# Kernel optimization log

Measured on AMD Instinct MI355X. Metric: run time of the kernel, lower is better.

Reference implementation:

```python
import jax, jax.numpy as jnp
import numpy as np

N_NODES = 100000
N_EDGES = 1600000
NODE_DIM = 3
EDGE_DIM = 32
HIDDEN = 128
OUT_DIM = 3
N_GRAPHS = 64


def _lin(key, fan_in, fan_out):
    k1, k2 = jax.random.split(key)
    s = 1.0 / np.sqrt(fan_in)
    W = jax.random.uniform(k1, (fan_in, fan_out), minval=-s, maxval=s, dtype=jnp.float32)
    b = jax.random.uniform(k2, (fan_out,), minval=-s, maxval=s, dtype=jnp.float32)
    return W, b


def setup_inputs() -> dict:
    key = jax.random.key(0)
    ks = jax.random.split(key, 16)
    x = jax.random.normal(ks[0], (N_NODES, NODE_DIM), dtype=jnp.float32)
    edge_index = jax.random.randint(ks[1], (2, N_EDGES), 0, N_NODES, dtype=jnp.int32)
    edge_attr = jax.random.normal(ks[2], (N_EDGES, EDGE_DIM), dtype=jnp.float32)
    batch = jnp.sort(jax.random.randint(ks[3], (N_NODES,), 0, N_GRAPHS, dtype=jnp.int32))
    # conv1: CGConv at channels=NODE_DIM, in = 2*NODE_DIM + EDGE_DIM
    Wf1, bf1 = _lin(ks[4], 2 * NODE_DIM + EDGE_DIM, NODE_DIM)
    Ws1, bs1 = _lin(ks[5], 2 * NODE_DIM + EDGE_DIM, NODE_DIM)
    Wp, bp = _lin(ks[6], NODE_DIM, HIDDEN)
    # two hidden CGConvs at channels=HIDDEN
    Wf2, bf2 = _lin(ks[7], 2 * HIDDEN + EDGE_DIM, HIDDEN)
    Ws2, bs2 = _lin(ks[8], 2 * HIDDEN + EDGE_DIM, HIDDEN)
    Wf3, bf3 = _lin(ks[9], 2 * HIDDEN + EDGE_DIM, HIDDEN)
    Ws3, bs3 = _lin(ks[10], 2 * HIDDEN + EDGE_DIM, HIDDEN)
    W1, b1 = _lin(ks[11], HIDDEN, HIDDEN)
    W2, b2 = _lin(ks[12], HIDDEN, OUT_DIM)
    return dict(x=x, edge_index=edge_index, edge_attr=edge_attr, batch=batch,
                Wf1=Wf1, bf1=bf1, Ws1=Ws1, bs1=bs1, Wp=Wp, bp=bp,
                Wf2=Wf2, bf2=bf2, Ws2=Ws2, bs2=bs2,
                Wf3=Wf3, bf3=bf3, Ws3=Ws3, bs3=bs3,
                W1=W1, b1=b1, W2=W2, b2=b2)


def _cgconv(x, src, dst, edge_attr, Wf, bf, Ws, bs):
    # z = [x_i (target), x_j (source), e_ij]; message = sigmoid(lin_f(z)) * softplus(lin_s(z))
    z = jnp.concatenate([x[dst], x[src], edge_attr], axis=-1)  # [E, 2C+F]
    m = jax.nn.sigmoid(z @ Wf + bf) * jax.nn.softplus(z @ Ws + bs)  # [E, C]
    agg = jax.ops.segment_sum(m, dst, num_segments=x.shape[0])
    return x + agg


def reference(x, edge_index, edge_attr, batch,
              Wf1, bf1, Ws1, bs1, Wp, bp,
              Wf2, bf2, Ws2, bs2, Wf3, bf3, Ws3, bs3,
              W1, b1, W2, b2):
    src, dst = edge_index[0], edge_index[1]
    h = _cgconv(x, src, dst, edge_attr, Wf1, bf1, Ws1, bs1)
    h = jax.nn.relu(h @ Wp + bp)
    h = jax.nn.relu(_cgconv(h, src, dst, edge_attr, Wf2, bf2, Ws2, bs2))
    h = jax.nn.relu(_cgconv(h, src, dst, edge_attr, Wf3, bf3, Ws3, bs3))
    # global mean pool over graphs
    sums = jax.ops.segment_sum(h, batch, num_segments=N_GRAPHS)
    counts = jax.ops.segment_sum(jnp.ones((h.shape[0],), h.dtype), batch, num_segments=N_GRAPHS)
    pooled = sums / jnp.maximum(counts, 1.0)[:, None]
    g = jax.nn.relu(pooled @ W1 + b1)
    return g @ W2 + b2
```

## Files before the change

### kernel.cpp

```cpp
#include <hip/hip_runtime.h>
#include <hip/hip_bf16.h>


#define N_NODES 100000
#define N_EDGES 1600000
#define HID 128
#define SCAN_BLOCKS 391

typedef unsigned int uint;
typedef short bf16x8 __attribute__((ext_vector_type(8)));
typedef float f32x4 __attribute__((ext_vector_type(4)));

__device__ inline float bflo(uint u) { return __uint_as_float(u << 16); }
__device__ inline float bfhi(uint u) { return __uint_as_float(u & 0xffff0000u); }
__device__ inline uint pack_bf16_2(float a, float b) {
  uint ua = __float_as_uint(a), ub = __float_as_uint(b);
  ua = (ua + 0x7fffu + ((ua >> 16) & 1u)) >> 16;
  ub = (ub + 0x7fffu + ((ub >> 16) & 1u)) >> 16;
  return ua | (ub << 16);
}
__device__ inline float sigmoidf_(float x) {
  return __builtin_amdgcn_rcpf(1.f + __expf(-x));
}
__device__ inline float softplusf_(float x) {
  return fmaxf(x, 0.f) + __logf(1.f + __expf(-fabsf(x)));
}

__global__ __launch_bounds__(256) void hist_k(const int* __restrict__ ei,
                                              int* __restrict__ deg) {
  int e = blockIdx.x * 256 + threadIdx.x;
  if (e >= N_EDGES) return;
  atomicAdd(&deg[ei[N_EDGES + e]], 1);
}

__global__ __launch_bounds__(256) void scan1_k(const int* __restrict__ deg,
                                               int* __restrict__ rowptr,
                                               int* __restrict__ bsums) {
  __shared__ int s[256];
  int i = blockIdx.x * 256 + threadIdx.x;
  int v = (i < N_NODES) ? deg[i] : 0;
  s[threadIdx.x] = v;
  __syncthreads();
  for (int off = 1; off < 256; off <<= 1) {
    int t = (threadIdx.x >= off) ? s[threadIdx.x - off] : 0;
    __syncthreads();
    s[threadIdx.x] += t;
    __syncthreads();
  }
  if (i < N_NODES) rowptr[i] = s[threadIdx.x] - v;
  if (threadIdx.x == 255) bsums[blockIdx.x] = s[255];
}

__global__ __launch_bounds__(512) void scan2_k(int* __restrict__ bsums) {
  __shared__ int s[512];
  int t = threadIdx.x;
  int v = (t < SCAN_BLOCKS) ? bsums[t] : 0;
  s[t] = v;
  __syncthreads();
  for (int off = 1; off < 512; off <<= 1) {
    int x = (t >= off) ? s[t - off] : 0;
    __syncthreads();
    s[t] += x;
    __syncthreads();
  }
  if (t < SCAN_BLOCKS) bsums[t] = s[t] - v;
}

__global__ __launch_bounds__(256) void scan3_k(int* __restrict__ rowptr,
                                               const int* __restrict__ bsums,
                                               int* __restrict__ cur) {
  int i = blockIdx.x * 256 + threadIdx.x;
  if (i < N_NODES) {
    int r = rowptr[i] + bsums[blockIdx.x];
    rowptr[i] = r;
    cur[i] = r;
  }
  if (i == 0) rowptr[N_NODES] = N_EDGES;
}

__global__ __launch_bounds__(256) void scatter_k(const int* __restrict__ ei,
                                                 int* __restrict__ cur,
                                                 uint4* __restrict__ csr) {
  int e = blockIdx.x * 256 + threadIdx.x;
  if (e >= N_EDGES) return;
  int d = ei[N_EDGES + e];
  int pos = atomicAdd(&cur[d], 1);
  csr[pos] = make_uint4((uint)ei[e], (uint)e, (uint)d, 0u);
}

__global__ __launch_bounds__(256) void ea_pack(const float* __restrict__ ea,
                                               const uint4* __restrict__ csr,
                                               uint4* __restrict__ eab) {
  long long t = (long long)blockIdx.x * 256 + threadIdx.x;
  int p = (int)(t >> 2), q = (int)(t & 3);
  if (p >= N_EDGES) return;
  uint e = csr[p].y;
  const float4* er = (const float4*)(ea + (long long)e * 32 + q * 8);
  float4 a0 = er[0], a1 = er[1];
  uint4 pk;
  pk.x = pack_bf16_2(a0.x, a0.y);
  pk.y = pack_bf16_2(a0.z, a0.w);
  pk.z = pack_bf16_2(a1.x, a1.y);
  pk.w = pack_bf16_2(a1.z, a1.w);
  eab[(long long)p * 4 + q] = pk;
}

__global__ __launch_bounds__(256) void conv1_edge(
    const float* __restrict__ x, const int* __restrict__ ei,
    const float* __restrict__ ea,
    const float* __restrict__ Wf, const float* __restrict__ bf,
    const float* __restrict__ Ws, const float* __restrict__ bs,
    float* __restrict__ agg1) {
  int e = blockIdx.x * 256 + threadIdx.x;
  if (e >= N_EDGES) return;
  int src = ei[e], dst = ei[N_EDGES + e];
  float z[38];
#pragma unroll
  for (int k = 0; k < 3; ++k) z[k] = x[dst * 3 + k];
#pragma unroll
  for (int k = 0; k < 3; ++k) z[3 + k] = x[src * 3 + k];
  const float4* er4 = (const float4*)(ea + (long long)e * 32);
#pragma unroll
  for (int k = 0; k < 8; ++k) {
    float4 v = er4[k];
    z[6 + 4 * k + 0] = v.x;
    z[6 + 4 * k + 1] = v.y;
    z[6 + 4 * k + 2] = v.z;
    z[6 + 4 * k + 3] = v.w;
  }
#pragma unroll
  for (int c = 0; c < 3; ++c) {
    float f = bf[c], s = bs[c];
#pragma unroll
    for (int k = 0; k < 38; ++k) {
      f = fmaf(z[k], Wf[k * 3 + c], f);
      s = fmaf(z[k], Ws[k * 3 + c], s);
    }
    atomicAdd(&agg1[dst * 3 + c], sigmoidf_(f) * softplusf_(s));
  }
}

__global__ __launch_bounds__(256) void proj2(
    const float* __restrict__ x, const float* __restrict__ agg1,
    const float* __restrict__ Wp, const float* __restrict__ bp,
    float* __restrict__ h, uint* __restrict__ hb) {
  long long i = (long long)blockIdx.x * 256 + threadIdx.x;
  if (i >= (long long)N_NODES * 64) return;
  int n = (int)(i >> 6), jp = (int)(i & 63);
  int j0 = jp * 2;
  float v0 = x[n * 3 + 0] + agg1[n * 3 + 0];
  float v1 = x[n * 3 + 1] + agg1[n * 3 + 1];
  float v2 = x[n * 3 + 2] + agg1[n * 3 + 2];
  float a0 = bp[j0], a1 = bp[j0 + 1];
  a0 = fmaf(v0, Wp[0 * HID + j0], a0);
  a0 = fmaf(v1, Wp[1 * HID + j0], a0);
  a0 = fmaf(v2, Wp[2 * HID + j0], a0);
  a1 = fmaf(v0, Wp[0 * HID + j0 + 1], a1);
  a1 = fmaf(v1, Wp[1 * HID + j0 + 1], a1);
  a1 = fmaf(v2, Wp[2 * HID + j0 + 1], a1);
  a0 = fmaxf(a0, 0.f);
  a1 = fmaxf(a1, 0.f);
  *(float2*)&h[(long long)n * HID + j0] = make_float2(a0, a1);
  hb[(long long)n * 64 + jp] = pack_bf16_2(a0, a1);
}

__global__ __launch_bounds__(256) void w_prep2(const float* __restrict__ Wf,
                                               const float* __restrict__ Ws,
                                               uint* __restrict__ Wpk) {
  int row = blockIdx.x * 256 + threadIdx.x;
  int pm = row >> 7;
  int c = row & 127;
  const float* W = (pm & 1) ? Ws : Wf;
  int rowoff = (pm >> 1) * 128;
  for (int kk = 0; kk < 64; ++kk) {
    float a = W[(rowoff + 2 * kk) * 128 + c];
    float b = W[(rowoff + 2 * kk + 1) * 128 + c];
    Wpk[row * 64 + kk] = pack_bf16_2(a, b);
  }
}

#define NG_STR 68
__global__ __launch_bounds__(256, 4) void node_gemmM(
    const uint* __restrict__ hb, const uint* __restrict__ Wpk,
    const float* __restrict__ bf, const float* __restrict__ bs,
    uint* __restrict__ Pb) {
  __shared__ uint Alds[64 * NG_STR];
  int part = blockIdx.x;
  int m0 = blockIdx.y * 64;
  int tid = threadIdx.x;
  {
    int r = tid >> 2, q = tid & 3;
    int row = m0 + r;
    uint* d = &Alds[r * NG_STR + q * 16];
    if (row < N_NODES) {
      const uint4* s4 = (const uint4*)&hb[(long long)row * 64 + q * 16];
      uint4 v0 = s4[0], v1 = s4[1], v2 = s4[2], v3 = s4[3];
      *(uint4*)(d + 0) = v0; *(uint4*)(d + 4) = v1;
      *(uint4*)(d + 8) = v2; *(uint4*)(d + 12) = v3;
    } else {
      uint4 z = make_uint4(0, 0, 0, 0);
      *(uint4*)(d + 0) = z; *(uint4*)(d + 4) = z;
      *(uint4*)(d + 8) = z; *(uint4*)(d + 12) = z;
    }
  }
  __syncthreads();
  int wave = tid >> 6, lane = tid & 63;
  int l15 = lane & 15, lq = lane >> 4;
  int arow = wave * 16 + l15;
  const uint* WpF = Wpk + (part * 2 + 0) * 128 * 64;
  const uint* WpS = Wpk + (part * 2 + 1) * 128 * 64;
  f32x4 accF[8], accS[8];
#pragma unroll
  for (int nt = 0; nt < 8; ++nt) {
    f32x4 z = {0.f, 0.f, 0.f, 0.f};
    accF[nt] = z;
    accS[nt] = z;
  }
#pragma unroll
  for (int ks = 0; ks < 4; ++ks) {
    bf16x8 afr = *(const bf16x8*)&Alds[arow * NG_STR + ks * 16 + lq * 4];
#pragma unroll
    for (int nt = 0; nt < 8; ++nt) {
      bf16x8 bF = *(const bf16x8*)&WpF[(nt * 16 + l15) * 64 + ks * 16 + lq * 4];
      bf16x8 bS = *(const bf16x8*)&WpS[(nt * 16 + l15) * 64 + ks * 16 + lq * 4];
      accF[nt] = __builtin_amdgcn_mfma_f32_16x16x32_bf16(afr, bF, accF[nt], 0, 0, 0);
      accS[nt] = __builtin_amdgcn_mfma_f32_16x16x32_bf16(afr, bS, accS[nt], 0, 0, 0);
    }
  }
#pragma unroll
  for (int nt = 0; nt < 8; ++nt) {
    int c = nt * 16 + l15;
    int pos = (nt >> 1) * 32 + l15 * 2 + (nt & 1);
    float fb = (part == 0) ? bf[c] : 0.f;
    float sb = (part == 0) ? bs[c] : 0.f;
#pragma unroll
    for (int reg = 0; reg < 4; ++reg) {
      int node = m0 + wave * 16 + lq * 4 + reg;
      if (node < N_NODES) {
        Pb[(long long)node * 256 + part * 128 + pos] =
            pack_bf16_2(accF[nt][reg] + fb, accS[nt][reg] + sb);
      }
    }
  }
}

__global__ __launch_bounds__(256) void w_prep(const float* __restrict__ Wf,
                                              const float* __restrict__ Ws,
                                              uint* __restrict__ Btg) {
  int t = threadIdx.x;
  const float* W = (t < 128) ? Wf : Ws;
  int c = t & 127;
#pragma unroll
  for (int kk = 0; kk < 16; ++kk) {
    float a = W[(256 + 2 * kk) * 128 + c];
    float b = W[(256 + 2 * kk + 1) * 128 + c];
    Btg[t * 16 + kk] = pack_bf16_2(a, b);
  }
}

#define EMSG_EB 64
#define CAP 16
__global__ __launch_bounds__(256, 7) void edge_msg(
    const uint* __restrict__ Pb, const uint* __restrict__ eab,
    const uint* __restrict__ Btg, const uint4* __restrict__ csr,
    const int* __restrict__ rowptr, float* __restrict__ h) {
  __shared__ float accL[CAP * 128];
  __shared__ int dstL[64], srcL[64], liL[64];
  __shared__ int dlist[CAP], compL[CAP];
  __shared__ int nDistS;
  int tid = threadIdx.x;
  int j0 = blockIdx.x * EMSG_EB;
#pragma unroll
  for (int i = 0; i < (CAP * 128) / 256; ++i) accL[tid + i * 256] = 0.f;
  if (tid < 64) {
    uint4 cj = csr[j0 + tid];
    int d = (int)cj.z;
    dstL[tid] = d;
    srcL[tid] = (int)cj.x;
    int dprev = __shfl_up(d, 1, 64);
    bool flag = (tid == 0) || (d != dprev);
    unsigned long long m = __ballot(flag);
    unsigned long long pre = (tid == 63) ? ~0ull : ((1ull << (tid + 1)) - 1);
    int li = __popcll(m & pre) - 1;
    liL[tid] = li;
    if (flag && li < CAP) {
      dlist[li] = d;
      int r0 = rowptr[d], r1 = rowptr[d + 1];
      compL[li] = ((r0 == j0 + tid) && (r1 <= j0 + EMSG_EB)) ? 1 : 0;
    }
    if (tid == 0) nDistS = __popcll(m);
  }
  __syncthreads();
  int wave = tid >> 6, lane = tid & 63;
  int c0w = wave * 32;
  int l15 = lane & 15, lq = lane >> 4;
  int chs0 = c0w + l15, chs1 = c0w + 16 + l15;
  int pbase = (wave << 5) + (l15 << 1);
  bf16x8 bfr0 = *(const bf16x8*)&Btg[chs0 * 16 + lq * 4];
  bf16x8 bfr1 = *(const bf16x8*)&Btg[chs1 * 16 + lq * 4];
  bf16x8 bfr2 = *(const bf16x8*)&Btg[(128 + chs0) * 16 + lq * 4];
  bf16x8 bfr3 = *(const bf16x8*)&Btg[(128 + chs1) * 16 + lq * 4];
#pragma unroll
  for (int mt = 0; mt < 4; ++mt) {
    bf16x8 afr =
        *(const bf16x8*)&eab[((long long)(j0 + mt * 16 + l15)) * 16 + lq * 4];
    f32x4 z = {0.f, 0.f, 0.f, 0.f};
    f32x4 accf0 = __builtin_amdgcn_mfma_f32_16x16x32_bf16(afr, bfr0, z, 0, 0, 0);
    f32x4 accf1 = __builtin_amdgcn_mfma_f32_16x16x32_bf16(afr, bfr1, z, 0, 0, 0);
    f32x4 accs0 = __builtin_amdgcn_mfma_f32_16x16x32_bf16(afr, bfr2, z, 0, 0, 0);
    f32x4 accs1 = __builtin_amdgcn_mfma_f32_16x16x32_bf16(afr, bfr3, z, 0, 0, 0);
    int o = mt * 16 + lq * 4;
    int dsts[4], lis[4];
#pragma unroll
    for (int reg = 0; reg < 4; ++reg) {
      dsts[reg] = dstL[o + reg];
      lis[reg] = liL[o + reg];
    }
    float mr0[4], mr1[4];
#pragma unroll
    for (int reg = 0; reg < 4; ++reg) {
      uint2 gd = *(const uint2*)&Pb[(long long)dsts[reg] * 256 + pbase];
      uint2 gs = *(const uint2*)&Pb[(long long)srcL[o + reg] * 256 + 128 + pbase];
      float f0 = accf0[reg] + bflo(gd.x) + bflo(gs.x);
      float s0 = accs0[reg] + bfhi(gd.x) + bfhi(gs.x);
      float f1 = accf1[reg] + bflo(gd.y) + bflo(gs.y);
      float s1 = accs1[reg] + bfhi(gd.y) + bfhi(gs.y);
      mr0[reg] = sigmoidf_(f0) * softplusf_(s0);
      mr1[reg] = sigmoidf_(f1) * softplusf_(s1);
    }
#pragma unroll
    for (int cp = 0; cp < 2; ++cp) {
      int c = (cp ? chs1 : chs0);
      const float* mr = cp ? mr1 : mr0;
      float racc = mr[0];
      int cl = lis[0], cd = dsts[0];
#pragma unroll
      for (int reg = 1; reg < 4; ++reg) {
        if (lis[reg] == cl) {
          racc += mr[reg];
        } else {
          if (cl < CAP) atomicAdd(&accL[cl * 128 + c], racc);
          else atomicAdd(&h[(long long)cd * HID + c], racc);
          cl = lis[reg]; cd = dsts[reg]; racc = mr[reg];
        }
      }
      if (cl < CAP) atomicAdd(&accL[cl * 128 + c], racc);
      else atomicAdd(&h[(long long)cd * HID + c], racc);
    }
  }
  __syncthreads();
  int nD = nDistS;
  if (nD > CAP) nD = CAP;
  int c = tid & 127;
  for (int li = tid >> 7; li < nD; li += 2) {
    int d = dlist[li];
    float v = accL[li * 128 + c];
    float* hp = &h[(long long)d * HID + c];
    if (compL[li]) {
      *hp = fmaxf(*hp + v, 0.f);
    } else {
      atomicAdd(hp, v);
    }
  }
}

__global__ __launch_bounds__(256) void relu2(float* __restrict__ h,
                                             uint* __restrict__ hb) {
  const int total = N_NODES * 32;
  for (int i = blockIdx.x * 256 + threadIdx.x; i < total; i += gridDim.x * 256) {
    float4 v = ((float4*)h)[i];
    v.x = fmaxf(v.x, 0.f); v.y = fmaxf(v.y, 0.f);
    v.z = fmaxf(v.z, 0.f); v.w = fmaxf(v.w, 0.f);
    ((float4*)h)[i] = v;
    uint2 o;
    o.x = pack_bf16_2(v.x, v.y);
    o.y = pack_bf16_2(v.z, v.w);
    *(uint2*)&hb[(long long)i * 2] = o;
  }
}

__global__ __launch_bounds__(256) void relu_k(float* __restrict__ h) {
  const int total = N_NODES * HID / 4;
  for (int i = blockIdx.x * 256 + threadIdx.x; i < total; i += gridDim.x * 256) {
    float4 v = ((float4*)h)[i];
    v.x = fmaxf(v.x, 0.f); v.y = fmaxf(v.y, 0.f);
    v.z = fmaxf(v.z, 0.f); v.w = fmaxf(v.w, 0.f);
    ((float4*)h)[i] = v;
  }
}

#define POOL_NODES 128
__global__ __launch_bounds__(128) void pool2(
    const float* __restrict__ h, const int* __restrict__ batch,
    float* __restrict__ sums, float* __restrict__ cnts) {
  int n0 = blockIdx.x * POOL_NODES;
  if (n0 >= N_NODES) return;
  int t = threadIdx.x;
  int nEnd = n0 + POOL_NODES;
  if (nEnd > N_NODES) nEnd = N_NODES;
  float acc = 0.f;
  int bcur = batch[n0];
  int cnt = 0;
  for (int n = n0; n < nEnd; ++n) {
    int b = batch[n];
    if (b != bcur) {
      atomicAdd(&sums[bcur * HID + t], acc);
      if (t == 0) atomicAdd(&cnts[bcur], (float)cnt);
      acc = 0.f; cnt = 0; bcur = b;
    }
    acc += h[(long long)n * HID + t];
    ++cnt;
  }
  atomicAdd(&sums[bcur * HID + t], acc);
  if (t == 0) atomicAdd(&cnts[bcur], (float)cnt);
}

__global__ __launch_bounds__(128) void mlpA(
    const float* __restrict__ sums, const float* __restrict__ cnts,
    const float* __restrict__ W1, const float* __restrict__ b1,
    float* __restrict__ g) {
  __shared__ float pl[HID];
  int gr = blockIdx.x, j = threadIdx.x;
  float cnt = fmaxf(cnts[gr], 1.f);
  pl[j] = sums[gr * HID + j] / cnt;
  __syncthreads();
  float acc = b1[j];
#pragma unroll 8
  for (int k = 0; k < HID; ++k) acc = fmaf(pl[k], W1[k * HID + j], acc);
  g[gr * HID + j] = fmaxf(acc, 0.f);
}

__global__ __launch_bounds__(256) void mlpB(
    const float* __restrict__ g, const float* __restrict__ W2,
    const float* __restrict__ b2, float* __restrict__ out) {
  int t = threadIdx.x;
  if (t >= 64 * 3) return;
  int gr = t / 3, o = t % 3;
  float acc = b2[o];
#pragma unroll 8
  for (int k = 0; k < HID; ++k) acc = fmaf(g[gr * HID + k], W2[k * 3 + o], acc);
  out[t] = acc;
}

extern "C" void kernel_launch(void* const* d_in, const int* in_sizes, int n_in,
                              void* d_out, int out_size, void* d_ws, size_t ws_size,
                              hipStream_t stream) {
  const float* x   = (const float*)d_in[0];
  const int*   ei  = (const int*)d_in[1];
  const float* ea  = (const float*)d_in[2];
  const int*   bat = (const int*)d_in[3];
  const float* Wf1 = (const float*)d_in[4];
  const float* bf1 = (const float*)d_in[5];
  const float* Ws1 = (const float*)d_in[6];
  const float* bs1 = (const float*)d_in[7];
  const float* Wp  = (const float*)d_in[8];
  const float* bp  = (const float*)d_in[9];
  const float* Wf2 = (const float*)d_in[10];
  const float* bf2 = (const float*)d_in[11];
  const float* Ws2 = (const float*)d_in[12];
  const float* bs2 = (const float*)d_in[13];
  const float* Wf3 = (const float*)d_in[14];
  const float* bf3 = (const float*)d_in[15];
  const float* Ws3 = (const float*)d_in[16];
  const float* bs3 = (const float*)d_in[17];
  const float* W1  = (const float*)d_in[18];
  const float* b1  = (const float*)d_in[19];
  const float* W2  = (const float*)d_in[20];
  const float* b2  = (const float*)d_in[21];
  float* out = (float*)d_out;

  char* w = (char*)d_ws;
  size_t off = 0;
  auto alloc = [&](size_t bytes) {
    void* p = w + off;
    off += (bytes + 255) & ~(size_t)255;
    return p;
  };
  int*   deg    = (int*)alloc((size_t)N_NODES * 4);
  int*   rowptr = (int*)alloc((size_t)(N_NODES + 1) * 4);
  int*   cur    = (int*)alloc((size_t)N_NODES * 4);
  int*   bsums  = (int*)alloc((size_t)512 * 4);
  uint4* csr    = (uint4*)alloc((size_t)N_EDGES * 16);
  float* agg1   = (float*)alloc((size_t)N_NODES * 3 * 4);
  float* h      = (float*)alloc((size_t)N_NODES * HID * 4);
  uint*  hb     = (uint*)alloc((size_t)N_NODES * 64 * 4);
  uint*  Pb     = (uint*)alloc((size_t)N_NODES * 256 * 4);
  uint*  eab    = (uint*)alloc((size_t)N_EDGES * 64);
  float* sums   = (float*)alloc((size_t)64 * HID * 4);
  float* cnts   = (float*)alloc((size_t)64 * 4);
  float* g      = (float*)alloc((size_t)64 * HID * 4);
  uint*  Btg    = (uint*)alloc((size_t)256 * 16 * 4);
  uint*  Wpk    = (uint*)alloc((size_t)512 * 64 * 4);
  (void)ws_size;

  hipMemsetAsync(deg, 0, (size_t)N_NODES * 4, stream);
  hist_k<<<(N_EDGES + 255) / 256, 256, 0, stream>>>(ei, deg);
  scan1_k<<<SCAN_BLOCKS, 256, 0, stream>>>(deg, rowptr, bsums);
  scan2_k<<<1, 512, 0, stream>>>(bsums);
  scan3_k<<<SCAN_BLOCKS, 256, 0, stream>>>(rowptr, bsums, cur);
  scatter_k<<<(N_EDGES + 255) / 256, 256, 0, stream>>>(ei, cur, csr);
  ea_pack<<<(N_EDGES * 4 + 255) / 256, 256, 0, stream>>>(ea, csr, (uint4*)eab);

  hipMemsetAsync(agg1, 0, (size_t)N_NODES * 3 * 4, stream);
  conv1_edge<<<(N_EDGES + 255) / 256, 256, 0, stream>>>(x, ei, ea, Wf1, bf1, Ws1, bs1, agg1);
  proj2<<<(N_NODES * 64 + 255) / 256, 256, 0, stream>>>(x, agg1, Wp, bp, h, hb);

  dim3 nggrid(2, (N_NODES + 63) / 64);
  int eblocks = N_EDGES / EMSG_EB;

  w_prep2<<<2, 256, 0, stream>>>(Wf2, Ws2, Wpk);
  node_gemmM<<<nggrid, 256, 0, stream>>>(hb, Wpk, bf2, bs2, Pb);
  w_prep<<<1, 256, 0, stream>>>(Wf2, Ws2, Btg);
  edge_msg<<<eblocks, 256, 0, stream>>>(Pb, eab, Btg, csr, rowptr, h);
  relu2<<<4096, 256, 0, stream>>>(h, hb);

  w_prep2<<<2, 256, 0, stream>>>(Wf3, Ws3, Wpk);
  node_gemmM<<<nggrid, 256, 0, stream>>>(hb, Wpk, bf3, bs3, Pb);
  w_prep<<<1, 256, 0, stream>>>(Wf3, Ws3, Btg);
  edge_msg<<<eblocks, 256, 0, stream>>>(Pb, eab, Btg, csr, rowptr, h);
  relu_k<<<4096, 256, 0, stream>>>(h);

  hipMemsetAsync(sums, 0, (size_t)(64 * HID + 64) * 4, stream);
  pool2<<<(N_NODES + POOL_NODES - 1) / POOL_NODES, POOL_NODES, 0, stream>>>(h, bat, sums, cnts);
  mlpA<<<64, 128, 0, stream>>>(sums, cnts, W1, b1, g);
  mlpB<<<1, 256, 0, stream>>>(g, W2, b2, out);
}
```

Baseline: 1.890 ms.

## Double edge tile per block in edge_msg and shrink pool tile

```diff
diff --git a/kernel.cpp b/kernel.cpp
--- a/kernel.cpp
+++ b/kernel.cpp
@@ -8,6 +8,7 @@
 #define SCAN_BLOCKS 391
 
 typedef unsigned int uint;
+typedef unsigned long long ull;
 typedef short bf16x8 __attribute__((ext_vector_type(8)));
 typedef float f32x4 __attribute__((ext_vector_type(4)));
 
@@ -258,37 +259,47 @@
   }
 }
 
-#define EMSG_EB 64
-#define CAP 16
+#define EMSG_EB 128
+#define CAP 24
 __global__ __launch_bounds__(256, 7) void edge_msg(
     const uint* __restrict__ Pb, const uint* __restrict__ eab,
     const uint* __restrict__ Btg, const uint4* __restrict__ csr,
     const int* __restrict__ rowptr, float* __restrict__ h) {
   __shared__ float accL[CAP * 128];
-  __shared__ int dstL[64], srcL[64], liL[64];
+  __shared__ int dstL[EMSG_EB], srcL[EMSG_EB], liL[EMSG_EB];
   __shared__ int dlist[CAP], compL[CAP];
-  __shared__ int nDistS;
+  __shared__ int nDistS, wcnt0S;
   int tid = threadIdx.x;
   int j0 = blockIdx.x * EMSG_EB;
 #pragma unroll
   for (int i = 0; i < (CAP * 128) / 256; ++i) accL[tid + i * 256] = 0.f;
-  if (tid < 64) {
+  int li_me = -1, d_me = 0;
+  bool flag = false;
+  ull mball = 0;
+  if (tid < EMSG_EB) {
     uint4 cj = csr[j0 + tid];
-    int d = (int)cj.z;
-    dstL[tid] = d;
+    d_me = (int)cj.z;
+    dstL[tid] = d_me;
     srcL[tid] = (int)cj.x;
-    int dprev = __shfl_up(d, 1, 64);
-    bool flag = (tid == 0) || (d != dprev);
-    unsigned long long m = __ballot(flag);
-    unsigned long long pre = (tid == 63) ? ~0ull : ((1ull << (tid + 1)) - 1);
-    int li = __popcll(m & pre) - 1;
-    liL[tid] = li;
-    if (flag && li < CAP) {
-      dlist[li] = d;
-      int r0 = rowptr[d], r1 = rowptr[d + 1];
-      compL[li] = ((r0 == j0 + tid) && (r1 <= j0 + EMSG_EB)) ? 1 : 0;
-    }
-    if (tid == 0) nDistS = __popcll(m);
+    int l = tid & 63;
+    int dp = __shfl_up(d_me, 1, 64);
+    int dprev = (l == 0) ? ((tid == 0) ? -1 : (int)csr[j0 + tid - 1].z) : dp;
+    flag = (d_me != dprev);
+    mball = __ballot(flag);
+    ull pre = (l == 63) ? ~0ull : ((1ull << (l + 1)) - 1);
+    li_me = __popcll(mball & pre) - 1;
+    if (tid == 0) wcnt0S = __popcll(mball);
+  }
+  __syncthreads();
+  if (tid >= 64 && tid < EMSG_EB) li_me += wcnt0S;
+  if (tid < EMSG_EB) {
+    liL[tid] = li_me;
+    if (flag && li_me < CAP) {
+      dlist[li_me] = d_me;
+      int r0 = rowptr[d_me], r1 = rowptr[d_me + 1];
+      compL[li_me] = ((r0 == j0 + tid) && (r1 <= j0 + EMSG_EB)) ? 1 : 0;
+    }
+    if (tid == 64) nDistS = wcnt0S + __popcll(mball);
   }
   __syncthreads();
   int wave = tid >> 6, lane = tid & 63;
@@ -301,7 +312,7 @@
   bf16x8 bfr2 = *(const bf16x8*)&Btg[(128 + chs0) * 16 + lq * 4];
   bf16x8 bfr3 = *(const bf16x8*)&Btg[(128 + chs1) * 16 + lq * 4];
 #pragma unroll
-  for (int mt = 0; mt < 4; ++mt) {
+  for (int mt = 0; mt < 8; ++mt) {
     bf16x8 afr =
         *(const bf16x8*)&eab[((long long)(j0 + mt * 16 + l15)) * 16 + lq * 4];
     f32x4 z = {0.f, 0.f, 0.f, 0.f};
@@ -389,7 +400,7 @@
   }
 }
 
-#define POOL_NODES 128
+#define POOL_NODES 32
 __global__ __launch_bounds__(128) void pool2(
     const float* __restrict__ h, const int* __restrict__ batch,
     float* __restrict__ sums, float* __restrict__ cnts) {
@@ -521,7 +532,7 @@
   relu_k<<<4096, 256, 0, stream>>>(h);
 
   hipMemsetAsync(sums, 0, (size_t)(64 * HID + 64) * 4, stream);
-  pool2<<<(N_NODES + POOL_NODES - 1) / POOL_NODES, POOL_NODES, 0, stream>>>(h, bat, sums, cnts);
+  pool2<<<(N_NODES + POOL_NODES - 1) / POOL_NODES, 128, 0, stream>>>(h, bat, sums, cnts);
   mlpA<<<64, 128, 0, stream>>>(sums, cnts, W1, b1, g);
   mlpB<<<1, 256, 0, stream>>>(g, W2, b2, out);
 }
```

Result: no change. 1.882 ms (-0.4%).
